# Optimization experiments

Hardware: AMD Instinct MI355X
Metric: run time of the kernel (lower is better)

Reference implementation:

```python
import jax, jax.numpy as jnp
import numpy as np

HIDDEN = 256
NUM_LEVELS = 4
BATCH = 256
NUM_SLOTS = 64
NUM_FEATURES = 4096


def setup_inputs() -> dict:
    key = jax.random.key(0)
    ks = jax.random.split(key, 6)
    s = 1.0 / np.sqrt(HIDDEN)
    return {
        "attention_weights": jax.random.uniform(ks[0], (BATCH, NUM_SLOTS, NUM_FEATURES), dtype=jnp.float32),
        "current_centers": jax.random.normal(ks[1], (NUM_FEATURES, HIDDEN), dtype=jnp.float32),
        "w_ih": jax.random.uniform(ks[2], (3 * HIDDEN, HIDDEN), jnp.float32, -s, s),
        "w_hh": jax.random.uniform(ks[3], (3 * HIDDEN, HIDDEN), jnp.float32, -s, s),
        "b_ih": jax.random.uniform(ks[4], (3 * HIDDEN,), jnp.float32, -s, s),
        "b_hh": jax.random.uniform(ks[5], (3 * HIDDEN,), jnp.float32, -s, s),
        "num_levels": NUM_LEVELS,
    }


def reference(attention_weights, current_centers, w_ih, w_hh, b_ih, b_hh, num_levels):
    B, S, F = attention_weights.shape
    H = current_centers.shape[1]
    O = S // num_levels  # num_objects

    # aggregated features: bmm with shared center matrix -> [B, S, H]
    x = jnp.einsum("bsf,fh->bsh", attention_weights, current_centers)

    # per-slot hidden state: slot i*L+j uses current_centers[i] -> [S, H]
    h = jnp.repeat(current_centers[:O], num_levels, axis=0)

    # fused GRUCell gates over all (batch, slot) pairs (torch gate order: r, z, n)
    gi = x @ w_ih.T + b_ih            # [B, S, 3H]
    gh = h @ w_hh.T + b_hh            # [S, 3H], broadcasts over batch
    gi_r, gi_z, gi_n = jnp.split(gi, 3, axis=-1)
    gh_r, gh_z, gh_n = jnp.split(gh, 3, axis=-1)

    r = jax.nn.sigmoid(gi_r + gh_r)
    z = jax.nn.sigmoid(gi_z + gh_z)
    n = jnp.tanh(gi_n + r * gh_n)
    h_new = (1.0 - z) * n + z * h     # [B, S, H]

    # average the num_levels updates per object, then stack objects first
    out = h_new.reshape(B, O, num_levels, H).mean(axis=2)  # [B, O, H]
    return jnp.transpose(out, (1, 0, 2))                   # [O, B, H]
```

## Files before the change

### kernel.cpp

```cpp
#include <hip/hip_runtime.h>
#include <stdint.h>


typedef _Float16 half8 __attribute__((ext_vector_type(8)));
typedef float f32x4 __attribute__((ext_vector_type(4)));

#define WS_CT   0u
#define WS_WP   2097152u
#define WS_GH   2490368u
#define WS_CSP  2686976u
#define WS_CS   2703360u
#define WS_CSW  2704384u
#define WS_X    2707456u

static __device__ __forceinline__ _Float16 f2h(float x) {
  return (_Float16)x;
}
static __device__ __forceinline__ void gload16(const void* g, void* lds) {
  __builtin_amdgcn_global_load_lds(
      (const __attribute__((address_space(1))) unsigned int*)g,
      (__attribute__((address_space(3))) unsigned int*)lds, 16, 0, 0);
}
static __device__ __forceinline__ float sigmf(float x) {
  float e = __expf(-fabsf(x));
  float p = 1.f / (1.f + e);
  return x >= 0.f ? p : 1.f - p;
}
static __device__ __forceinline__ float tanhf2(float x) {
  float e = __expf(-2.f * fabsf(x));
  float t = 1.f - 2.f * e / (1.f + e);
  return x >= 0.f ? t : -t;
}

__global__ void __launch_bounds__(256) k_transC(const float* __restrict__ C,
                                                _Float16* __restrict__ Ct) {
  __shared__ float sT[64][65];
  const int f0 = blockIdx.x * 64, h0 = blockIdx.y * 64;
  const int t = threadIdx.x;
#pragma unroll
  for (int i = 0; i < 4; ++i) {
    int fl = t + 256 * i;
    int r = fl >> 4, c4 = fl & 15;
    float4 v = *(const float4*)(C + (size_t)(f0 + r) * 256 + h0 + c4 * 4);
    sT[r][c4 * 4 + 0] = v.x; sT[r][c4 * 4 + 1] = v.y;
    sT[r][c4 * 4 + 2] = v.z; sT[r][c4 * 4 + 3] = v.w;
  }
  __syncthreads();
#pragma unroll
  for (int i = 0; i < 2; ++i) {
    int q = t + 256 * i;
    int hr = q >> 3, j = q & 7;
    int h = h0 + hr;
    union { half8 v; _Float16 u[8]; } pk;
#pragma unroll
    for (int u = 0; u < 8; ++u) pk.u[u] = f2h(sT[j * 8 + u][hr]);
    size_t off = (size_t)h * 8192 + (size_t)f0 * 2 + (size_t)((j ^ (h & 7)) << 4);
    *(half8*)((char*)Ct + off) = pk.v;
  }
}

__global__ void __launch_bounds__(256) k_csum(const float* __restrict__ C,
                                              float* __restrict__ part) {
  const int b = blockIdx.x, t = threadIdx.x;
  float s = 0.f;
  for (int k = 0; k < 256; ++k) s += C[(size_t)(b * 256 + k) * 256 + t];
  part[b * 256 + t] = s;
}
__global__ void __launch_bounds__(256) k_csum2(const float* __restrict__ part,
                                               float* __restrict__ csum) {
  const int t = threadIdx.x;
  float s = 0.f;
#pragma unroll
  for (int b = 0; b < 16; ++b) s += part[b * 256 + t];
  csum[t] = 0.5f * s;
}
__global__ void __launch_bounds__(256) k_csumW(const float* __restrict__ w_ih,
                                               const float* __restrict__ cs,
                                               float* __restrict__ csW) {
  const int n = blockIdx.x * 256 + threadIdx.x;
  float s = 0.f;
  for (int h = 0; h < 256; ++h) s += cs[h] * w_ih[(size_t)n * 256 + h];
  csW[n] = s;
}

__global__ void __launch_bounds__(256) k_prepWp(const float* __restrict__ w_ih,
                                                _Float16* __restrict__ Wp) {
  int q = blockIdx.x * 256 + threadIdx.x;
  int row = q >> 5, c = q & 31;
  int seg = c >> 3, j = c & 7;
  int srow = (row % 3) * 256 + row / 3;
  const float* src = w_ih + (size_t)srow * 256 + c * 8;
  union { half8 v; _Float16 u[8]; } pk;
#pragma unroll
  for (int u = 0; u < 8; ++u) pk.u[u] = f2h(src[u]);
  size_t off = (size_t)row * 512 + seg * 128 + ((j ^ (row & 7)) << 4);
  *(half8*)((char*)Wp + off) = pk.v;
}

__global__ void __launch_bounds__(256) k_gh(const float* __restrict__ centers,
                                            const float* __restrict__ w_hh,
                                            const float* __restrict__ b_hh,
                                            float* __restrict__ GH) {
  __shared__ __align__(16) float sH[256];
  const int s = blockIdx.x, t = threadIdx.x;
  sH[t] = centers[(size_t)(s >> 2) * 256 + t];
  __syncthreads();
#pragma unroll
  for (int e = 0; e < 3; ++e) {
    int n = e * 256 + t;
    float accv = b_hh[n];
    const float4* w = (const float4*)(w_hh + (size_t)n * 256);
#pragma unroll 8
    for (int k = 0; k < 64; ++k) {
      float4 v = w[k];
      float4 hh = *(const float4*)&sH[k * 4];
      accv += v.x * hh.x + v.y * hh.y + v.z * hh.z + v.w * hh.w;
    }
    GH[(size_t)s * 768 + n] = accv;
  }
}

__global__ void __launch_bounds__(256) k_stage1(const float* __restrict__ A,
                                                const _Float16* __restrict__ Ct,
                                                _Float16* __restrict__ X) {
  __shared__ __align__(16) _Float16 sA[32 * 64];
  __shared__ __align__(16) _Float16 sB[2][256 * 64];
  const int t = threadIdx.x;
  const int wid = t >> 6, l = t & 63;
  const int lr = l & 15, lk = l >> 4;
  const int m0 = blockIdx.x * 32;

  f32x4 acc[2][4];
#pragma unroll
  for (int i = 0; i < 2; ++i)
#pragma unroll
    for (int j = 0; j < 4; ++j) acc[i][j] = (f32x4){0.f, 0.f, 0.f, 0.f};

  const int ar = t >> 3, aj = t & 7;
  const float* aptr = A + (size_t)(m0 + ar) * 4096 + aj * 8;
  const int saw = ar * 128 + ((aj ^ (ar & 7)) << 4);

  const int br = t >> 3, bj = t & 7;

  f32x4 a0 = __builtin_nontemporal_load((const f32x4*)(aptr));
  f32x4 a1 = __builtin_nontemporal_load((const f32x4*)(aptr + 4));
#pragma unroll
  for (int i = 0; i < 8; ++i) {
    gload16(Ct + (size_t)(br + 32 * i) * 4096 + bj * 8,
            (char*)&sB[0][0] + (wid * 64 + 256 * i) * 16);
  }
  asm volatile("s_waitcnt vmcnt(0)" ::: "memory");

#pragma unroll 2
  for (int kk = 0; kk < 64; ++kk) {
    const int cur = kk & 1;
    {
      union { half8 v; _Float16 u[8]; } pk;
      pk.u[0] = f2h(a0.x - 0.5f); pk.u[1] = f2h(a0.y - 0.5f);
      pk.u[2] = f2h(a0.z - 0.5f); pk.u[3] = f2h(a0.w - 0.5f);
      pk.u[4] = f2h(a1.x - 0.5f); pk.u[5] = f2h(a1.y - 0.5f);
      pk.u[6] = f2h(a1.z - 0.5f); pk.u[7] = f2h(a1.w - 0.5f);
      *(half8*)((char*)sA + saw) = pk.v;
    }
    f32x4 n0, n1;
    if (kk < 63) {
      const float* ap = aptr + (kk + 1) * 64;
      n0 = __builtin_nontemporal_load((const f32x4*)(ap));
      n1 = __builtin_nontemporal_load((const f32x4*)(ap + 4));
#pragma unroll
      for (int i = 0; i < 8; ++i) {
        gload16(Ct + (size_t)(br + 32 * i) * 4096 + (size_t)(kk + 1) * 64 + bj * 8,
                (char*)&sB[cur ^ 1][0] + (wid * 64 + 256 * i) * 16);
      }
    }
    asm volatile("s_waitcnt lgkmcnt(0)" ::: "memory");
    __builtin_amdgcn_s_barrier();
    asm volatile("" ::: "memory");

    const char* pA = (const char*)sA;
    const char* pB = (const char*)&sB[cur][0];
#pragma unroll
    for (int kc = 0; kc < 2; ++kc) {
      const int q = kc * 4 + lk;
      half8 af[2];
#pragma unroll
      for (int mi = 0; mi < 2; ++mi) {
        int rl = mi * 16 + lr;
        af[mi] = *(const half8*)(pA + rl * 128 + ((q ^ (rl & 7)) << 4));
      }
#pragma unroll
      for (int ni = 0; ni < 4; ++ni) {
        int rb = wid * 64 + ni * 16 + lr;
        half8 bf = *(const half8*)(pB + rb * 128 + ((q ^ (rb & 7)) << 4));
#pragma unroll
        for (int mi = 0; mi < 2; ++mi)
          acc[mi][ni] = __builtin_amdgcn_mfma_f32_16x16x32_f16(af[mi], bf, acc[mi][ni], 0, 0, 0);
      }
    }
    __syncthreads();
    if (kk < 63) { a0 = n0; a1 = n1; }
  }

#pragma unroll
  for (int mi = 0; mi < 2; ++mi)
#pragma unroll
    for (int ni = 0; ni < 4; ++ni)
#pragma unroll
      for (int p = 0; p < 4; ++p) {
        int m = m0 + mi * 16 + lk * 4 + p;
        int col = wid * 64 + ni * 16 + lr;
        size_t off = (size_t)m * 512 + ((col >> 6) << 7) +
                     ((((col >> 3) & 7) ^ (m & 7)) << 4) + ((col & 7) << 1);
        *(_Float16*)((char*)X + off) = f2h(acc[mi][ni][p]);
      }
}

__global__ void __launch_bounds__(256) k_stage2(const _Float16* __restrict__ X,
                                                const _Float16* __restrict__ Wp,
                                                const float* __restrict__ GH,
                                                const float* __restrict__ centers,
                                                const float* __restrict__ b_ih,
                                                const float* __restrict__ csW,
                                                float* __restrict__ out) {
  __shared__ __align__(16) char smem[81920];
  _Float16* sX = (_Float16*)smem;
  char*     sW = smem + 32768;
  float*    sC = (float*)(smem + 32768);
  const int t = threadIdx.x;
  const int wid = t >> 6, l = t & 63;
  const int lr = l & 15, lk = l >> 4;
  const int wm = wid >> 1, wn = wid & 1;
  const int b = blockIdx.x;

#pragma unroll
  for (int i = 0; i < 8; ++i) {
    int flat = t + 256 * i;
    gload16((const char*)X + ((size_t)b * 64 + (flat >> 5)) * 512 +
                (size_t)(flat & 31) * 16,
            (char*)sX + (wid * 64 + 256 * i) * 16);
  }
  __syncthreads();

  for (int nt = 0; nt < 8; ++nt) {
    const int n0 = nt * 96;
    f32x4 acc[2][3];
#pragma unroll
    for (int i = 0; i < 2; ++i)
#pragma unroll
      for (int j = 0; j < 3; ++j) acc[i][j] = (f32x4){0.f, 0.f, 0.f, 0.f};

#pragma unroll
    for (int i = 0; i < 12; ++i) {
      int flat = t + 256 * i;
      gload16((const char*)Wp + (size_t)(n0 + (flat >> 5)) * 512 +
                  (size_t)(flat & 31) * 16,
              sW + (wid * 64 + 256 * i) * 16);
    }
    __syncthreads();
#pragma unroll
    for (int kc = 0; kc < 8; ++kc) {
      const int q = kc * 4 + lk;
      const int seg = (q >> 3) << 7, jj = q & 7;
      half8 af[2];
#pragma unroll
      for (int mi = 0; mi < 2; ++mi) {
        int rl = wm * 32 + mi * 16 + lr;
        af[mi] = *(const half8*)((const char*)sX + rl * 512 + seg + ((jj ^ (rl & 7)) << 4));
      }
#pragma unroll
      for (int ni = 0; ni < 3; ++ni) {
        int rw = wn * 48 + ni * 16 + lr;
        half8 bf = *(const half8*)(sW + rw * 512 + seg + ((jj ^ (rw & 7)) << 4));
#pragma unroll
        for (int mi = 0; mi < 2; ++mi)
          acc[mi][ni] = __builtin_amdgcn_mfma_f32_16x16x32_f16(af[mi], bf, acc[mi][ni], 0, 0, 0);
      }
    }
    __syncthreads();
#pragma unroll
    for (int mi = 0; mi < 2; ++mi)
#pragma unroll
      for (int ni = 0; ni < 3; ++ni)
#pragma unroll
        for (int p = 0; p < 4; ++p) {
          int row = wm * 32 + mi * 16 + lk * 4 + p;
          int col = wn * 48 + ni * 16 + lr;
          sC[row * 100 + col] = acc[mi][ni][p];
        }
    __syncthreads();
#pragma unroll
    for (int ii = 0; ii < 2; ++ii) {
      int item = t + 256 * ii;
      int hl = item & 31, o = item >> 5;
      int h = nt * 32 + hl;
      float hprev = centers[o * 256 + h];
      float bir = b_ih[h] + csW[h];
      float biz = b_ih[256 + h] + csW[256 + h];
      float bin = b_ih[512 + h] + csW[512 + h];
      float sum = 0.f;
#pragma unroll
      for (int j = 0; j < 4; ++j) {
        int s = 4 * o + j;
        float gir = sC[s * 100 + 3 * hl + 0] + bir;
        float giz = sC[s * 100 + 3 * hl + 1] + biz;
        float gin = sC[s * 100 + 3 * hl + 2] + bin;
        float rg = sigmf(gir + GH[s * 768 + h]);
        float zg = sigmf(giz + GH[s * 768 + 256 + h]);
        float ng = tanhf2(gin + rg * GH[s * 768 + 512 + h]);
        sum += (1.f - zg) * ng + zg * hprev;
      }
      out[(size_t)o * 65536 + (size_t)b * 256 + h] = 0.25f * sum;
    }
    __syncthreads();
  }
}

extern "C" void kernel_launch(void* const* d_in, const int* in_sizes, int n_in,
                              void* d_out, int out_size, void* d_ws, size_t ws_size,
                              hipStream_t stream) {
  (void)in_sizes; (void)n_in; (void)out_size; (void)ws_size;
  const float* attn    = (const float*)d_in[0];
  const float* centers = (const float*)d_in[1];
  const float* w_ih    = (const float*)d_in[2];
  const float* w_hh    = (const float*)d_in[3];
  const float* b_ih    = (const float*)d_in[4];
  const float* b_hh    = (const float*)d_in[5];

  char* ws = (char*)d_ws;
  _Float16* Ct  = (_Float16*)(ws + WS_CT);
  _Float16* Wpp = (_Float16*)(ws + WS_WP);
  float*    GHp = (float*)(ws + WS_GH);
  float*    csp = (float*)(ws + WS_CSP);
  float*    cs  = (float*)(ws + WS_CS);
  float*    csW = (float*)(ws + WS_CSW);
  _Float16* X   = (_Float16*)(ws + WS_X);
  float* out = (float*)d_out;

  hipLaunchKernelGGL(k_transC, dim3(64, 4), dim3(256), 0, stream, centers, Ct);
  hipLaunchKernelGGL(k_csum, dim3(16), dim3(256), 0, stream, centers, csp);
  hipLaunchKernelGGL(k_csum2, dim3(1), dim3(256), 0, stream, csp, cs);
  hipLaunchKernelGGL(k_csumW, dim3(3), dim3(256), 0, stream, w_ih, cs, csW);
  hipLaunchKernelGGL(k_prepWp, dim3(96), dim3(256), 0, stream, w_ih, Wpp);
  hipLaunchKernelGGL(k_gh, dim3(64), dim3(256), 0, stream, centers, w_hh, b_hh, GHp);
  hipLaunchKernelGGL(k_stage1, dim3(512), dim3(256), 0, stream, attn, Ct, X);
  hipLaunchKernelGGL(k_stage2, dim3(256), dim3(256), 0, stream, X, Wpp, GHp, centers, b_ih, csW, out);
}
```

Measured before the change: 179.8 us.

## Double M tile in stage1 GEMM and triple-buffer B with prefetch distance two

The stage1 GEMM block now covers 64 rows with 512 threads arranged as 2x4 waves, so each Ct tile loaded into shared memory is reused across twice as many A rows. B tiles move to a three-stage ring buffer and A tiles to double buffers, prefetched two k-steps ahead. A partial vmcnt wait replaces the full drain, and one barrier per iteration replaces two. This aims to hide global load latency and halve Ct traffic, at the cost of more LDS per block (about 112KB), which likely limits each CU to one block and a grid of only 256 blocks.

```diff
diff --git a/kernel.cpp b/kernel.cpp
--- a/kernel.cpp
+++ b/kernel.cpp
@@ -120,15 +120,16 @@
   }
 }
 
-__global__ void __launch_bounds__(256) k_stage1(const float* __restrict__ A,
+__global__ void __launch_bounds__(512) k_stage1(const float* __restrict__ A,
                                                 const _Float16* __restrict__ Ct,
                                                 _Float16* __restrict__ X) {
-  __shared__ __align__(16) _Float16 sA[32 * 64];
-  __shared__ __align__(16) _Float16 sB[2][256 * 64];
+  __shared__ __align__(16) _Float16 sA[2][64 * 64];
+  __shared__ __align__(16) _Float16 sB[3][256 * 64];
   const int t = threadIdx.x;
   const int wid = t >> 6, l = t & 63;
   const int lr = l & 15, lk = l >> 4;
-  const int m0 = blockIdx.x * 32;
+  const int wm = wid >> 2, wn = wid & 3;
+  const int m0 = blockIdx.x * 64;
 
   f32x4 acc[2][4];
 #pragma unroll
@@ -142,63 +143,79 @@
 
   const int br = t >> 3, bj = t & 7;
 
-  f32x4 a0 = __builtin_nontemporal_load((const f32x4*)(aptr));
-  f32x4 a1 = __builtin_nontemporal_load((const f32x4*)(aptr + 4));
-#pragma unroll
-  for (int i = 0; i < 8; ++i) {
-    gload16(Ct + (size_t)(br + 32 * i) * 4096 + bj * 8,
-            (char*)&sB[0][0] + (wid * 64 + 256 * i) * 16);
-  }
-  asm volatile("s_waitcnt vmcnt(0)" ::: "memory");
-
-#pragma unroll 2
+  f32x4 t0 = __builtin_nontemporal_load((const f32x4*)(aptr));
+  f32x4 t1 = __builtin_nontemporal_load((const f32x4*)(aptr + 4));
+  f32x4 p0 = __builtin_nontemporal_load((const f32x4*)(aptr + 64));
+  f32x4 p1 = __builtin_nontemporal_load((const f32x4*)(aptr + 64 + 4));
+#pragma unroll
+  for (int i = 0; i < 4; ++i) {
+    size_t so = (size_t)(br + 64 * i) * 4096 + bj * 8;
+    int db = (wid * 64 + 512 * i) * 16;
+    gload16(Ct + so, (char*)&sB[0][0] + db);
+    gload16(Ct + (size_t)64 + so, (char*)&sB[1][0] + db);
+  }
+  {
+    union { half8 v; _Float16 u[8]; } pk;
+    pk.u[0] = f2h(t0.x - 0.5f); pk.u[1] = f2h(t0.y - 0.5f);
+    pk.u[2] = f2h(t0.z - 0.5f); pk.u[3] = f2h(t0.w - 0.5f);
+    pk.u[4] = f2h(t1.x - 0.5f); pk.u[5] = f2h(t1.y - 0.5f);
+    pk.u[6] = f2h(t1.z - 0.5f); pk.u[7] = f2h(t1.w - 0.5f);
+    *(half8*)((char*)&sA[0][0] + saw) = pk.v;
+  }
+
+  int bcur = 0, bnxt = 2;
   for (int kk = 0; kk < 64; ++kk) {
-    const int cur = kk & 1;
-    {
-      union { half8 v; _Float16 u[8]; } pk;
-      pk.u[0] = f2h(a0.x - 0.5f); pk.u[1] = f2h(a0.y - 0.5f);
-      pk.u[2] = f2h(a0.z - 0.5f); pk.u[3] = f2h(a0.w - 0.5f);
-      pk.u[4] = f2h(a1.x - 0.5f); pk.u[5] = f2h(a1.y - 0.5f);
-      pk.u[6] = f2h(a1.z - 0.5f); pk.u[7] = f2h(a1.w - 0.5f);
-      *(half8*)((char*)sA + saw) = pk.v;
-    }
-    f32x4 n0, n1;
     if (kk < 63) {
-      const float* ap = aptr + (kk + 1) * 64;
-      n0 = __builtin_nontemporal_load((const f32x4*)(ap));
-      n1 = __builtin_nontemporal_load((const f32x4*)(ap + 4));
-#pragma unroll
-      for (int i = 0; i < 8; ++i) {
-        gload16(Ct + (size_t)(br + 32 * i) * 4096 + (size_t)(kk + 1) * 64 + bj * 8,
-                (char*)&sB[cur ^ 1][0] + (wid * 64 + 256 * i) * 16);
-      }
+      asm volatile("s_waitcnt vmcnt(6)" ::: "memory");
+    } else {
+      asm volatile("s_waitcnt vmcnt(0)" ::: "memory");
     }
     asm volatile("s_waitcnt lgkmcnt(0)" ::: "memory");
     __builtin_amdgcn_s_barrier();
-    asm volatile("" ::: "memory");
-
-    const char* pA = (const char*)sA;
-    const char* pB = (const char*)&sB[cur][0];
+
+    f32x4 q0, q1;
+    if (kk < 62) {
+      const float* ap = aptr + (kk + 2) * 64;
+      q0 = __builtin_nontemporal_load((const f32x4*)(ap));
+      q1 = __builtin_nontemporal_load((const f32x4*)(ap + 4));
+#pragma unroll
+      for (int i = 0; i < 4; ++i) {
+        size_t so = (size_t)(br + 64 * i) * 4096 + (size_t)(kk + 2) * 64 + bj * 8;
+        gload16(Ct + so, (char*)&sB[bnxt][0] + (wid * 64 + 512 * i) * 16);
+      }
+    }
+    if (kk < 63) {
+      union { half8 v; _Float16 u[8]; } pk;
+      pk.u[0] = f2h(p0.x - 0.5f); pk.u[1] = f2h(p0.y - 0.5f);
+      pk.u[2] = f2h(p0.z - 0.5f); pk.u[3] = f2h(p0.w - 0.5f);
+      pk.u[4] = f2h(p1.x - 0.5f); pk.u[5] = f2h(p1.y - 0.5f);
+      pk.u[6] = f2h(p1.z - 0.5f); pk.u[7] = f2h(p1.w - 0.5f);
+      *(half8*)((char*)&sA[(kk + 1) & 1][0] + saw) = pk.v;
+    }
+
+    const char* pA = (const char*)&sA[kk & 1][0];
+    const char* pB = (const char*)&sB[bcur][0];
 #pragma unroll
     for (int kc = 0; kc < 2; ++kc) {
       const int q = kc * 4 + lk;
       half8 af[2];
 #pragma unroll
       for (int mi = 0; mi < 2; ++mi) {
-        int rl = mi * 16 + lr;
+        int rl = wm * 32 + mi * 16 + lr;
         af[mi] = *(const half8*)(pA + rl * 128 + ((q ^ (rl & 7)) << 4));
       }
 #pragma unroll
       for (int ni = 0; ni < 4; ++ni) {
-        int rb = wid * 64 + ni * 16 + lr;
+        int rb = wn * 64 + ni * 16 + lr;
         half8 bf = *(const half8*)(pB + rb * 128 + ((q ^ (rb & 7)) << 4));
 #pragma unroll
         for (int mi = 0; mi < 2; ++mi)
           acc[mi][ni] = __builtin_amdgcn_mfma_f32_16x16x32_f16(af[mi], bf, acc[mi][ni], 0, 0, 0);
       }
     }
-    __syncthreads();
-    if (kk < 63) { a0 = n0; a1 = n1; }
+    if (kk < 62) { p0 = q0; p1 = q1; }
+    bcur = (bcur == 2) ? 0 : bcur + 1;
+    bnxt = (bnxt == 2) ? 0 : bnxt + 1;
   }
 
 #pragma unroll
@@ -207,8 +224,8 @@
     for (int ni = 0; ni < 4; ++ni)
 #pragma unroll
       for (int p = 0; p < 4; ++p) {
-        int m = m0 + mi * 16 + lk * 4 + p;
-        int col = wid * 64 + ni * 16 + lr;
+        int m = m0 + wm * 32 + mi * 16 + lk * 4 + p;
+        int col = wn * 64 + ni * 16 + lr;
         size_t off = (size_t)m * 512 + ((col >> 6) << 7) +
                      ((((col >> 3) & 7) ^ (m & 7)) << 4) + ((col & 7) << 1);
         *(_Float16*)((char*)X + off) = f2h(acc[mi][ni][p]);
@@ -342,6 +359,6 @@
   hipLaunchKernelGGL(k_csumW, dim3(3), dim3(256), 0, stream, w_ih, cs, csW);
   hipLaunchKernelGGL(k_prepWp, dim3(96), dim3(256), 0, stream, w_ih, Wpp);
   hipLaunchKernelGGL(k_gh, dim3(64), dim3(256), 0, stream, centers, w_hh, b_hh, GHp);
-  hipLaunchKernelGGL(k_stage1, dim3(512), dim3(256), 0, stream, attn, Ct, X);
+  hipLaunchKernelGGL(k_stage1, dim3(256), dim3(512), 0, stream, attn, Ct, X);
   hipLaunchKernelGGL(k_stage2, dim3(256), dim3(256), 0, stream, X, Wpp, GHp, centers, b_ih, csW, out);
 }
```

Result: no change. 181.5 us (+0.9%).

## Enlarge stage1 M tile to 64, prefetch A two steps ahead, parallelize reductions

Applied to the files above, without the earlier changes.

Stage1 now processes 64 rows per block instead of 32, doubling reuse of each B tile loaded into LDS and halving total B traffic. A is prefetched two k-steps ahead into register sets with double-buffered LDS tiles, and the trailing barrier is a bare s_barrier. The small center-sum and csW reductions are spread over more blocks, with csW using a wave shuffle reduction. In exchange the grid halves to 256 blocks, each with more accumulator registers and about 80KB of LDS, so occupancy drops.

```diff
diff --git a/kernel.cpp b/kernel.cpp
--- a/kernel.cpp
+++ b/kernel.cpp
@@ -9,9 +9,9 @@
 #define WS_WP   2097152u
 #define WS_GH   2490368u
 #define WS_CSP  2686976u
-#define WS_CS   2703360u
-#define WS_CSW  2704384u
-#define WS_X    2707456u
+#define WS_CS   2752512u
+#define WS_CSW  2753536u
+#define WS_X    2756608u
 
 static __device__ __forceinline__ _Float16 f2h(float x) {
   return (_Float16)x;
@@ -63,7 +63,7 @@
                                               float* __restrict__ part) {
   const int b = blockIdx.x, t = threadIdx.x;
   float s = 0.f;
-  for (int k = 0; k < 256; ++k) s += C[(size_t)(b * 256 + k) * 256 + t];
+  for (int k = 0; k < 64; ++k) s += C[(size_t)(b * 64 + k) * 256 + t];
   part[b * 256 + t] = s;
 }
 __global__ void __launch_bounds__(256) k_csum2(const float* __restrict__ part,
@@ -71,16 +71,20 @@
   const int t = threadIdx.x;
   float s = 0.f;
 #pragma unroll
-  for (int b = 0; b < 16; ++b) s += part[b * 256 + t];
+  for (int b = 0; b < 64; ++b) s += part[b * 256 + t];
   csum[t] = 0.5f * s;
 }
 __global__ void __launch_bounds__(256) k_csumW(const float* __restrict__ w_ih,
                                                const float* __restrict__ cs,
                                                float* __restrict__ csW) {
-  const int n = blockIdx.x * 256 + threadIdx.x;
-  float s = 0.f;
-  for (int h = 0; h < 256; ++h) s += cs[h] * w_ih[(size_t)n * 256 + h];
-  csW[n] = s;
+  const int wv = threadIdx.x >> 6, l = threadIdx.x & 63;
+  const int n = blockIdx.x * 4 + wv;
+  float4 w = *(const float4*)(w_ih + (size_t)n * 256 + l * 4);
+  float4 c = *(const float4*)(cs + l * 4);
+  float s = w.x * c.x + w.y * c.y + w.z * c.z + w.w * c.w;
+#pragma unroll
+  for (int off = 32; off; off >>= 1) s += __shfl_down(s, off, 64);
+  if (l == 0) csW[n] = s;
 }
 
 __global__ void __launch_bounds__(256) k_prepWp(const float* __restrict__ w_ih,
@@ -120,89 +124,106 @@
   }
 }
 
-__global__ void __launch_bounds__(256) k_stage1(const float* __restrict__ A,
-                                                const _Float16* __restrict__ Ct,
-                                                _Float16* __restrict__ X) {
-  __shared__ __align__(16) _Float16 sA[32 * 64];
-  __shared__ __align__(16) _Float16 sB[2][256 * 64];
+__global__ void __launch_bounds__(256, 1) k_stage1(const float* __restrict__ A,
+                                                   const _Float16* __restrict__ Ct,
+                                                   _Float16* __restrict__ X) {
+  __shared__ __align__(16) _Float16 sA0[64 * 64];
+  __shared__ __align__(16) _Float16 sA1[64 * 64];
+  __shared__ __align__(16) _Float16 sB0[256 * 64];
+  __shared__ __align__(16) _Float16 sB1[256 * 64];
   const int t = threadIdx.x;
   const int wid = t >> 6, l = t & 63;
   const int lr = l & 15, lk = l >> 4;
-  const int m0 = blockIdx.x * 32;
-
-  f32x4 acc[2][4];
-#pragma unroll
-  for (int i = 0; i < 2; ++i)
+  const int m0 = blockIdx.x * 64;
+
+  f32x4 acc[4][4];
+#pragma unroll
+  for (int i = 0; i < 4; ++i)
 #pragma unroll
     for (int j = 0; j < 4; ++j) acc[i][j] = (f32x4){0.f, 0.f, 0.f, 0.f};
 
-  const int ar = t >> 3, aj = t & 7;
-  const float* aptr = A + (size_t)(m0 + ar) * 4096 + aj * 8;
-  const int saw = ar * 128 + ((aj ^ (ar & 7)) << 4);
-
-  const int br = t >> 3, bj = t & 7;
-
-  f32x4 a0 = __builtin_nontemporal_load((const f32x4*)(aptr));
-  f32x4 a1 = __builtin_nontemporal_load((const f32x4*)(aptr + 4));
-#pragma unroll
-  for (int i = 0; i < 8; ++i) {
-    gload16(Ct + (size_t)(br + 32 * i) * 4096 + bj * 8,
-            (char*)&sB[0][0] + (wid * 64 + 256 * i) * 16);
-  }
-  asm volatile("s_waitcnt vmcnt(0)" ::: "memory");
-
-#pragma unroll 2
-  for (int kk = 0; kk < 64; ++kk) {
-    const int cur = kk & 1;
+  const int ar = t >> 2, ac4 = t & 3;
+  const float* aptr = A + (size_t)(m0 + ar) * 4096 + ac4 * 16;
+  const int saw0 = ar * 128 + (((2 * ac4 + 0) ^ (ar & 7)) << 4);
+  const int saw1 = ar * 128 + (((2 * ac4 + 1) ^ (ar & 7)) << 4);
+
+  const int brow = t >> 3, bch = t & 7;
+
+#pragma unroll
+  for (int i = 0; i < 8; ++i)
+    gload16(Ct + (size_t)(brow + 32 * i) * 4096 + bch * 8,
+            (char*)sB0 + (wid * 64 + 256 * i) * 16);
+  f32x4 aEv[4], aOd[4];
+#pragma unroll
+  for (int j = 0; j < 4; ++j)
+    aEv[j] = __builtin_nontemporal_load((const f32x4*)(aptr + j * 4));
+#pragma unroll
+  for (int j = 0; j < 4; ++j)
+    aOd[j] = __builtin_nontemporal_load((const f32x4*)(aptr + 64 + j * 4));
+
+  auto ITER = [&](int kk, f32x4* areg, _Float16* sAc, _Float16* sBc,
+                  _Float16* sBn) {
+    asm volatile("s_waitcnt vmcnt(0)" ::: "memory");
     {
-      union { half8 v; _Float16 u[8]; } pk;
-      pk.u[0] = f2h(a0.x - 0.5f); pk.u[1] = f2h(a0.y - 0.5f);
-      pk.u[2] = f2h(a0.z - 0.5f); pk.u[3] = f2h(a0.w - 0.5f);
-      pk.u[4] = f2h(a1.x - 0.5f); pk.u[5] = f2h(a1.y - 0.5f);
-      pk.u[6] = f2h(a1.z - 0.5f); pk.u[7] = f2h(a1.w - 0.5f);
-      *(half8*)((char*)sA + saw) = pk.v;
-    }
-    f32x4 n0, n1;
-    if (kk < 63) {
-      const float* ap = aptr + (kk + 1) * 64;
-      n0 = __builtin_nontemporal_load((const f32x4*)(ap));
-      n1 = __builtin_nontemporal_load((const f32x4*)(ap + 4));
-#pragma unroll
-      for (int i = 0; i < 8; ++i) {
-        gload16(Ct + (size_t)(br + 32 * i) * 4096 + (size_t)(kk + 1) * 64 + bj * 8,
-                (char*)&sB[cur ^ 1][0] + (wid * 64 + 256 * i) * 16);
-      }
+      union { half8 v; _Float16 u[8]; } w0, w1;
+      w0.u[0] = f2h(areg[0].x - 0.5f); w0.u[1] = f2h(areg[0].y - 0.5f);
+      w0.u[2] = f2h(areg[0].z - 0.5f); w0.u[3] = f2h(areg[0].w - 0.5f);
+      w0.u[4] = f2h(areg[1].x - 0.5f); w0.u[5] = f2h(areg[1].y - 0.5f);
+      w0.u[6] = f2h(areg[1].z - 0.5f); w0.u[7] = f2h(areg[1].w - 0.5f);
+      w1.u[0] = f2h(areg[2].x - 0.5f); w1.u[1] = f2h(areg[2].y - 0.5f);
+      w1.u[2] = f2h(areg[2].z - 0.5f); w1.u[3] = f2h(areg[2].w - 0.5f);
+      w1.u[4] = f2h(areg[3].x - 0.5f); w1.u[5] = f2h(areg[3].y - 0.5f);
+      w1.u[6] = f2h(areg[3].z - 0.5f); w1.u[7] = f2h(areg[3].w - 0.5f);
+      *(half8*)((char*)sAc + saw0) = w0.v;
+      *(half8*)((char*)sAc + saw1) = w1.v;
+    }
+    if (kk <= 61) {
+      const float* ap = aptr + (kk + 2) * 64;
+#pragma unroll
+      for (int j = 0; j < 4; ++j)
+        areg[j] = __builtin_nontemporal_load((const f32x4*)(ap + j * 4));
+    }
+    if (kk <= 62) {
+#pragma unroll
+      for (int i = 0; i < 8; ++i)
+        gload16(Ct + (size_t)(brow + 32 * i) * 4096 + (size_t)(kk + 1) * 64 + bch * 8,
+                (char*)sBn + (wid * 64 + 256 * i) * 16);
     }
     asm volatile("s_waitcnt lgkmcnt(0)" ::: "memory");
     __builtin_amdgcn_s_barrier();
     asm volatile("" ::: "memory");
-
-    const char* pA = (const char*)sA;
-    const char* pB = (const char*)&sB[cur][0];
 #pragma unroll
     for (int kc = 0; kc < 2; ++kc) {
       const int q = kc * 4 + lk;
-      half8 af[2];
-#pragma unroll
-      for (int mi = 0; mi < 2; ++mi) {
+      half8 af[4], bf[4];
+#pragma unroll
+      for (int mi = 0; mi < 4; ++mi) {
         int rl = mi * 16 + lr;
-        af[mi] = *(const half8*)(pA + rl * 128 + ((q ^ (rl & 7)) << 4));
+        af[mi] = *(const half8*)((const char*)sAc + rl * 128 + ((q ^ (rl & 7)) << 4));
       }
 #pragma unroll
       for (int ni = 0; ni < 4; ++ni) {
         int rb = wid * 64 + ni * 16 + lr;
-        half8 bf = *(const half8*)(pB + rb * 128 + ((q ^ (rb & 7)) << 4));
-#pragma unroll
-        for (int mi = 0; mi < 2; ++mi)
-          acc[mi][ni] = __builtin_amdgcn_mfma_f32_16x16x32_f16(af[mi], bf, acc[mi][ni], 0, 0, 0);
-      }
-    }
-    __syncthreads();
-    if (kk < 63) { a0 = n0; a1 = n1; }
-  }
-
-#pragma unroll
-  for (int mi = 0; mi < 2; ++mi)
+        bf[ni] = *(const half8*)((const char*)sBc + rb * 128 + ((q ^ (rb & 7)) << 4));
+      }
+#pragma unroll
+      for (int mi = 0; mi < 4; ++mi)
+#pragma unroll
+        for (int ni = 0; ni < 4; ++ni)
+          acc[mi][ni] = __builtin_amdgcn_mfma_f32_16x16x32_f16(af[mi], bf[ni], acc[mi][ni], 0, 0, 0);
+    }
+    asm volatile("" ::: "memory");
+    __builtin_amdgcn_s_barrier();
+    asm volatile("" ::: "memory");
+  };
+
+  for (int kx = 0; kx < 64; kx += 2) {
+    ITER(kx + 0, aEv, sA0, sB0, sB1);
+    ITER(kx + 1, aOd, sA1, sB1, sB0);
+  }
+
+#pragma unroll
+  for (int mi = 0; mi < 4; ++mi)
 #pragma unroll
     for (int ni = 0; ni < 4; ++ni)
 #pragma unroll
@@ -337,11 +358,11 @@
   float* out = (float*)d_out;
 
   hipLaunchKernelGGL(k_transC, dim3(64, 4), dim3(256), 0, stream, centers, Ct);
-  hipLaunchKernelGGL(k_csum, dim3(16), dim3(256), 0, stream, centers, csp);
+  hipLaunchKernelGGL(k_csum, dim3(64), dim3(256), 0, stream, centers, csp);
   hipLaunchKernelGGL(k_csum2, dim3(1), dim3(256), 0, stream, csp, cs);
-  hipLaunchKernelGGL(k_csumW, dim3(3), dim3(256), 0, stream, w_ih, cs, csW);
+  hipLaunchKernelGGL(k_csumW, dim3(192), dim3(256), 0, stream, w_ih, cs, csW);
   hipLaunchKernelGGL(k_prepWp, dim3(96), dim3(256), 0, stream, w_ih, Wpp);
   hipLaunchKernelGGL(k_gh, dim3(64), dim3(256), 0, stream, centers, w_hh, b_hh, GHp);
-  hipLaunchKernelGGL(k_stage1, dim3(512), dim3(256), 0, stream, attn, Ct, X);
+  hipLaunchKernelGGL(k_stage1, dim3(256), dim3(256), 0, stream, attn, Ct, X);
   hipLaunchKernelGGL(k_stage2, dim3(256), dim3(256), 0, stream, X, Wpp, GHp, centers, b_ih, csW, out);
 }
```

Measured after the change: 195.6 us. 1.09x slower.
